# Optimization experiments

Measured on AMD Instinct MI355X. Metric: run time of the kernel, lower is better.

## Reference

```python
import jax, jax.numpy as jnp
import numpy as np

N_NODES = 100000
N_EDGES = 3200000
N_GRAPHS = 64
NEG_SLOPE = 0.2


def mish(x):
    return x * jnp.tanh(jax.nn.softplus(x))


def gat_layer(x, src, dst, W, b, a_src, a_dst, heads, out_ch, n_nodes):
    # h: [N, H, C]
    h = (x @ W).reshape(n_nodes, heads, out_ch)
    alpha_s = jnp.sum(h * a_src[None], axis=-1)  # [N, H]
    alpha_d = jnp.sum(h * a_dst[None], axis=-1)  # [N, H]
    e = jax.nn.leaky_relu(alpha_s[src] + alpha_d[dst], NEG_SLOPE)  # [E, H]
    # scatter-softmax over incoming edges of each destination node
    emax = jax.ops.segment_max(e, dst, num_segments=n_nodes)  # [N, H]
    ee = jnp.exp(e - emax[dst])
    den = jax.ops.segment_sum(ee, dst, num_segments=n_nodes)
    alpha = ee / (den[dst] + 1e-16)  # [E, H]
    msg = h[src] * alpha[..., None]  # [E, H, C]
    out = jax.ops.segment_sum(msg, dst, num_segments=n_nodes)
    return out.reshape(n_nodes, heads * out_ch) + b


def setup_inputs() -> dict:
    key = jax.random.key(0)
    ks = jax.random.split(key, 10)
    x = jax.random.normal(ks[0], (N_NODES, 128), dtype=jnp.float32)
    edge_index = jax.random.randint(ks[1], (2, N_EDGES), 0, N_NODES, dtype=jnp.int64)
    batch = jnp.sort(jax.random.randint(ks[2], (N_NODES,), 0, N_GRAPHS, dtype=jnp.int64))
    s1 = 1.0 / np.sqrt(128.0)
    s2 = 1.0 / np.sqrt(16.0)
    return {
        "x": x,
        "edge_index": edge_index,
        "batch": batch,
        "W1": jax.random.normal(ks[3], (128, 16), dtype=jnp.float32) * s1,
        "b1": jnp.zeros((16,), dtype=jnp.float32),
        "a_src1": jax.random.normal(ks[4], (4, 4), dtype=jnp.float32) * 0.5,
        "a_dst1": jax.random.normal(ks[5], (4, 4), dtype=jnp.float32) * 0.5,
        "W2": jax.random.normal(ks[6], (16, 32), dtype=jnp.float32) * s2,
        "b2": jnp.zeros((32,), dtype=jnp.float32),
        "a_src2": jax.random.normal(ks[7], (1, 32), dtype=jnp.float32) * 0.5,
        "a_dst2": jax.random.normal(ks[8], (1, 32), dtype=jnp.float32) * 0.5,
    }


def reference(x, edge_index, batch, W1, b1, a_src1, a_dst1, W2, b2, a_src2, a_dst2):
    n = x.shape[0]
    # PyG GATConv default add_self_loops=True
    loop = jnp.arange(n, dtype=edge_index.dtype)
    src = jnp.concatenate([edge_index[0], loop])
    dst = jnp.concatenate([edge_index[1], loop])
    h = mish(gat_layer(x, src, dst, W1, b1, a_src1, a_dst1, heads=4, out_ch=4, n_nodes=n))
    h = mish(gat_layer(h, src, dst, W2, b2, a_src2, a_dst2, heads=1, out_ch=32, n_nodes=n))
    # global_mean_pool
    sums = jax.ops.segment_sum(h, batch, num_segments=N_GRAPHS)
    cnts = jax.ops.segment_sum(jnp.ones((n,), h.dtype), batch, num_segments=N_GRAPHS)
    return sums / jnp.maximum(cnts, 1.0)[:, None]
```

## Files before the change

### kernel.cpp

```cpp
#include <hip/hip_runtime.h>
#include <hip/hip_fp16.h>
#include <math.h>

#define NEG_SLOPE 0.2f
#define GB 192
#define SB 320
#define CHMAX 11264
#define CAP 5120
#define CAPH 2560

typedef _Float16 half2v __attribute__((ext_vector_type(2)));
typedef _Float16 half4v __attribute__((ext_vector_type(4)));

__device__ __forceinline__ float mishf(float x) {
    if (x > 15.f) return x;
    float ex = __expf(x);
    float y = 1.f + ex;
    float y2 = y * y;
    return x * (y2 - 1.f) / (y2 + 1.f);
}

__device__ __forceinline__ float lw(float e) {
    return __expf(fmaxf(e, NEG_SLOPE * e));
}

__device__ __forceinline__ float hdot2a(half2v a, half2v b, float c) {
#if __has_builtin(__builtin_amdgcn_fdot2)
    return __builtin_amdgcn_fdot2(a, b, c, false);
#else
    return (float)a.x * (float)b.x + (float)a.y * (float)b.y + c;
#endif
}

__global__ __launch_bounds__(1024) void front_kernel(
        const float* __restrict__ x, const float* __restrict__ W1,
        const float* __restrict__ a_dst,
        const float* __restrict__ W2, const float* __restrict__ as2,
        const float* __restrict__ ad2,
        _Float16* __restrict__ hpre1h, float* __restrict__ addst,
        float* __restrict__ vs, float* __restrict__ vd,
        const int* __restrict__ src, const int* __restrict__ dst,
        int E, int Etot, int CH, int NB, int N, int NT,
        int* __restrict__ cursor, int* __restrict__ pairs) {
    __shared__ __attribute__((aligned(16))) char smem[63824];
    int tid = threadIdx.x;
    if (blockIdx.x < GB) {
        float* Wlt = (float*)smem;
        float* xs  = Wlt + 16 * 132;
        if (blockIdx.x == 0 && tid < 16) {
            float ps = 0.f, pd = 0.f;
            #pragma unroll
            for (int c = 0; c < 32; c++) {
                float w = W2[tid * 32 + c];
                ps += w * as2[c];
                pd += w * ad2[c];
            }
            vs[tid] = ps; vd[tid] = pd;
        }
        for (int i = tid; i < 2048; i += 1024) Wlt[(i & 15) * 132 + (i >> 4)] = W1[i];
        int nl = tid >> 4, ch = tid & 15;
        for (int t = blockIdx.x; t < NT; t += GB) {
            int nodebase = t * 64;
            int nvalid = min(64, N - nodebase);
            __syncthreads();
            const float4* x4 = (const float4*)(x + (size_t)nodebase * 128);
            #pragma unroll
            for (int u = 0; u < 2; u++) {
                int i = tid + (u << 10);
                int tnl = i >> 5;
                if (tnl < nvalid) {
                    float4 v = x4[i];
                    int k = (i & 31) * 4;
                    float* dp = &xs[tnl * 132 + k];
                    dp[0] = v.x; dp[1] = v.y; dp[2] = v.z; dp[3] = v.w;
                }
            }
            __syncthreads();
            if (nl < nvalid) {
                const float4* xr4 = (const float4*)&xs[nl * 132];
                const float4* wr4 = (const float4*)&Wlt[ch * 132];
                float acc = 0.f;
                #pragma unroll
                for (int k4 = 0; k4 < 32; k4++) {
                    float4 xv = xr4[k4];
                    float4 wv = wr4[k4];
                    acc += xv.x * wv.x + xv.y * wv.y + xv.z * wv.z + xv.w * wv.w;
                }
                int node = nodebase + nl;
                hpre1h[node * 16 + ch] = (_Float16)acc;
                float pd = acc * a_dst[ch];
                pd += __shfl_xor(pd, 1); pd += __shfl_xor(pd, 2);
                if ((ch & 3) == 0) addst[node * 4 + (ch >> 2)] = pd;
            }
        }
    } else {
        int nb2 = 2 * NB;
        int* A    = (int*)smem;
        int* Boff = A + nb2;
        int* C    = Boff + nb2;
        int* buf  = C + nb2;
        int blk = blockIdx.x - GB;
        for (int b = tid; b < nb2; b += 1024) A[b] = 0;
        __syncthreads();
        int ibeg = blk * CH, iend = min((blk + 1) * CH, Etot);
        int cdv[11], cs[11];
        #pragma unroll
        for (int u = 0; u < 11; u++) {
            int i = ibeg + tid + (u << 10);
            int d = -1, s = 0;
            if (i < iend) {
                if (i < E) { d = dst[i]; s = src[i]; } else { d = i - E; s = d; }
                atomicAdd(&A[d >> 6], 1);
            }
            cdv[u] = d; cs[u] = s;
        }
        for (int i = ibeg + CHMAX + tid; i < iend; i += 1024) {
            int d, s;
            if (i < E) { d = dst[i]; s = src[i]; } else { d = i - E; s = d; }
            int f = d >> 6;
            int pos = atomicAdd(&cursor[f], 1);
            pos = pos < CAPH ? pos : CAPH - 1;
            size_t addr = (size_t)(f >> 1) * CAP + ((f & 1) ? (CAP - 1 - pos) : pos);
            pairs[addr] = s | ((d & 63) << 17);
        }
        __syncthreads();
        for (int b = tid; b < nb2; b += 1024) Boff[b] = A[b];
        __syncthreads();
        for (int o = 1; o < nb2; o <<= 1) {
            int i1 = tid, i2 = tid + 1024;
            int v1 = 0, v2 = 0;
            if (i1 < nb2 && i1 >= o) v1 = Boff[i1 - o];
            if (i2 < nb2 && i2 >= o) v2 = Boff[i2 - o];
            __syncthreads();
            if (i1 < nb2) Boff[i1] += v1;
            if (i2 < nb2) Boff[i2] += v2;
            __syncthreads();
        }
        for (int b = tid; b < nb2; b += 1024) {
            int cnt = A[b];
            Boff[b] -= cnt;
            C[b] = cnt ? atomicAdd(&cursor[b], cnt) : 0;
        }
        __syncthreads();
        for (int b = tid; b < nb2; b += 1024) A[b] = 0;
        __syncthreads();
        #pragma unroll
        for (int u = 0; u < 11; u++) {
            int d = cdv[u];
            if (d < 0) continue;
            int f = d >> 6;
            int r = atomicAdd(&A[f], 1);
            buf[Boff[f] + r] = cs[u] | ((d & 63) << 17);
        }
        __syncthreads();
        int total = iend - ibeg;
        if (total > CHMAX) total = CHMAX;
        if (total < 0) total = 0;
        for (int j = tid; j < total; j += 1024) {
            int lo = 0, hi = nb2 - 1;
            while (lo < hi) {
                int mid = (lo + hi + 1) >> 1;
                if (Boff[mid] <= j) lo = mid; else hi = mid - 1;
            }
            int f = lo;
            int pos = C[f] + (j - Boff[f]);
            pos = pos < CAPH ? pos : CAPH - 1;
            size_t addr = (size_t)(f >> 1) * CAP + ((f & 1) ? (CAP - 1 - pos) : pos);
            pairs[addr] = buf[j];
        }
    }
}

__global__ __launch_bounds__(256) void csragg1_kernel(
        const int* __restrict__ pairs, const int* __restrict__ btotal,
        int NB, int N,
        int* __restrict__ ssorted, int* __restrict__ rs, int* __restrict__ re,
        const float* __restrict__ a_src1, const float* __restrict__ addst,
        const _Float16* __restrict__ hpre1h, const float* __restrict__ b1,
        const float* __restrict__ vs, const float* __restrict__ vd,
        _Float16* __restrict__ hpack,
        float* __restrict__ ad2n) {
    __shared__ int deg[64];
    __shared__ int s[64];
    __shared__ int cur[64];
    __shared__ __attribute__((aligned(16))) int lds_sorted[CAPH];
    int tid = threadIdx.x, bh = blockIdx.x;
    int B = bh >> 1, half = bh & 1;
    int nb0 = (B << 7) + (half << 6);
    int cnt_nodes = min(64, N - nb0);
    int c = min(btotal[bh], CAPH);
    int rbase = B * CAP + (half ? CAP - c : 0);
    if (tid < 64) deg[tid] = 0;
    __syncthreads();
    for (int j = tid; j < c; j += 256)
        atomicAdd(&deg[(pairs[rbase + j] >> 17) & 63], 1);
    __syncthreads();
    if (tid < 64) s[tid] = deg[tid];
    __syncthreads();
    for (int o = 1; o < 64; o <<= 1) {
        int v = 0;
        if (tid < 64 && tid >= o) v = s[tid - o];
        __syncthreads();
        if (tid < 64) s[tid] += v;
        __syncthreads();
    }
    if (tid < 64) {
        int ex = s[tid] - deg[tid];
        cur[tid] = ex;
        if (tid < cnt_nodes) {
            rs[nb0 + tid] = bh * CAPH + ex;
            re[nb0 + tid] = bh * CAPH + ex + deg[tid];
        }
    }
    __syncthreads();
    for (int j = tid; j < c; j += 256) {
        int p = pairs[rbase + j];
        int pos = atomicAdd(&cur[(p >> 17) & 63], 1);
        lds_sorted[pos < CAPH ? pos : CAPH - 1] = p & 0x1FFFF;
    }
    __syncthreads();

    {
        int t4 = c >> 2;
        const int4* ls4 = (const int4*)lds_sorted;
        int4* gs4 = (int4*)(ssorted + (size_t)bh * CAPH);
        for (int j = tid; j < t4; j += 256) gs4[j] = ls4[j];
        for (int j = (t4 << 2) + tid; j < c; j += 256)
            ssorted[(size_t)bh * CAPH + j] = lds_sorted[j];
    }

    int wave = tid >> 6;
    int lane = tid & 63;
    int head = lane & 3, er = lane >> 2;
    int c0 = head * 4;
    half2v w01, w23;
    w01.x = (_Float16)a_src1[c0];     w01.y = (_Float16)a_src1[c0 + 1];
    w23.x = (_Float16)a_src1[c0 + 2]; w23.y = (_Float16)a_src1[c0 + 3];
    for (int r = 0; r < 16; r++) {
        int ln = (wave << 4) + r;
        if (ln >= cnt_nodes) break;
        int node = nb0 + ln;
        int end = cur[ln];
        int start = end - deg[ln];
        float adh = addst[node * 4 + head];
        float den = 0.f, a0 = 0.f, a1 = 0.f, a2 = 0.f, a3 = 0.f;
        int last = end - 1;
        int jb = start;
        for (; jb + 32 <= end; jb += 32) {
            int s0 = lds_sorted[jb + er];
            int s1 = lds_sorted[jb + 16 + er];
            half4v h0 = *(const half4v*)(hpre1h + (size_t)s0 * 16 + c0);
            half4v h1 = *(const half4v*)(hpre1h + (size_t)s1 * 16 + c0);
            half2v h0lo = __builtin_shufflevector(h0, h0, 0, 1);
            half2v h0hi = __builtin_shufflevector(h0, h0, 2, 3);
            half2v h1lo = __builtin_shufflevector(h1, h1, 0, 1);
            half2v h1hi = __builtin_shufflevector(h1, h1, 2, 3);
            float p0 = hdot2a(h0lo, w01, hdot2a(h0hi, w23, 0.f));
            float p1 = hdot2a(h1lo, w01, hdot2a(h1hi, w23, 0.f));
            float wt0 = lw(p0 + adh);
            float wt1 = lw(p1 + adh);
            den += wt0 + wt1;
            a0 += (float)h0.x * wt0 + (float)h1.x * wt1;
            a1 += (float)h0.y * wt0 + (float)h1.y * wt1;
            a2 += (float)h0.z * wt0 + (float)h1.z * wt1;
            a3 += (float)h0.w * wt0 + (float)h1.w * wt1;
        }
        if (jb < end) {
            int j0 = jb + er, j1 = jb + 16 + er;
            int k0 = (j0 <= last) ? j0 : last;
            int k1 = (j1 <= last) ? j1 : last;
            int s0 = lds_sorted[k0];
            int s1 = lds_sorted[k1];
            half4v h0 = *(const half4v*)(hpre1h + (size_t)s0 * 16 + c0);
            half4v h1 = *(const half4v*)(hpre1h + (size_t)s1 * 16 + c0);
            half2v h0lo = __builtin_shufflevector(h0, h0, 0, 1);
            half2v h0hi = __builtin_shufflevector(h0, h0, 2, 3);
            half2v h1lo = __builtin_shufflevector(h1, h1, 0, 1);
            half2v h1hi = __builtin_shufflevector(h1, h1, 2, 3);
            float p0 = hdot2a(h0lo, w01, hdot2a(h0hi, w23, 0.f));
            float p1 = hdot2a(h1lo, w01, hdot2a(h1hi, w23, 0.f));
            float wt0 = (j0 <= last) ? lw(p0 + adh) : 0.f;
            float wt1 = (j1 <= last) ? lw(p1 + adh) : 0.f;
            den += wt0 + wt1;
            a0 += (float)h0.x * wt0 + (float)h1.x * wt1;
            a1 += (float)h0.y * wt0 + (float)h1.y * wt1;
            a2 += (float)h0.z * wt0 + (float)h1.z * wt1;
            a3 += (float)h0.w * wt0 + (float)h1.w * wt1;
        }
        a0 += __shfl_xor(a0, 4);  a1 += __shfl_xor(a1, 4);  a2 += __shfl_xor(a2, 4);  a3 += __shfl_xor(a3, 4);  den += __shfl_xor(den, 4);
        a0 += __shfl_xor(a0, 8);  a1 += __shfl_xor(a1, 8);  a2 += __shfl_xor(a2, 8);  a3 += __shfl_xor(a3, 8);  den += __shfl_xor(den, 8);
        a0 += __shfl_xor(a0, 16); a1 += __shfl_xor(a1, 16); a2 += __shfl_xor(a2, 16); a3 += __shfl_xor(a3, 16); den += __shfl_xor(den, 16);
        a0 += __shfl_xor(a0, 32); a1 += __shfl_xor(a1, 32); a2 += __shfl_xor(a2, 32); a3 += __shfl_xor(a3, 32); den += __shfl_xor(den, 32);
        if (er == 0) {
            float inv = 1.f / (den + 1e-16f);
            float o0 = mishf(a0 * inv + b1[c0]);
            float o1 = mishf(a1 * inv + b1[c0 + 1]);
            float o2 = mishf(a2 * inv + b1[c0 + 2]);
            float o3 = mishf(a3 * inv + b1[c0 + 3]);
            half4v oh;
            oh.x = (_Float16)o0; oh.y = (_Float16)o1;
            oh.z = (_Float16)o2; oh.w = (_Float16)o3;
            _Float16* rec = hpack + (size_t)node * 32;
            *(half4v*)(rec + c0) = oh;
            float ps = o0 * vs[c0] + o1 * vs[c0 + 1] + o2 * vs[c0 + 2] + o3 * vs[c0 + 3];
            float pd = o0 * vd[c0] + o1 * vd[c0 + 1] + o2 * vd[c0 + 2] + o3 * vd[c0 + 3];
            ps += __shfl_xor(ps, 1); pd += __shfl_xor(pd, 1);
            ps += __shfl_xor(ps, 2); pd += __shfl_xor(pd, 2);
            if (head == 0) {
                *(float*)(rec + 16) = ps;
                ad2n[node] = pd;
            }
        }
    }
}

__global__ void agg2_kernel(const int* __restrict__ rs, const int* __restrict__ re,
                            const int* __restrict__ ssorted,
                            const _Float16* __restrict__ hpack,
                            const float* __restrict__ ad2n,
                            float* __restrict__ agg16, float* __restrict__ denv, int N) {
    int wave = threadIdx.x >> 6;
    int lane = threadIdx.x & 63;
    int b = blockIdx.x;
    int xcd = b & 7, i = b >> 3;
    int f = xcd + ((i >> 4) << 3);
    int sub = i & 15;
    int node = f * 64 + sub * 4 + wave;
    if (node >= N) return;
    int start = rs[node], end = re[node];
    int q = lane & 3, er = lane >> 2;
    int c0 = q * 4;
    float adh = ad2n[node];
    float den = 0.f, a0 = 0.f, a1 = 0.f, a2 = 0.f, a3 = 0.f;
    int last = end - 1;
    int jb = start;
    for (; jb + 32 <= end; jb += 32) {
        int s0 = __builtin_nontemporal_load(ssorted + jb + er);
        int s1 = __builtin_nontemporal_load(ssorted + jb + 16 + er);
        const _Float16* r0 = hpack + (size_t)s0 * 32;
        const _Float16* r1 = hpack + (size_t)s1 * 32;
        float as0 = *(const float*)(r0 + 16);
        float as1 = *(const float*)(r1 + 16);
        half4v h0 = *(const half4v*)(r0 + c0);
        half4v h1 = *(const half4v*)(r1 + c0);
        float wt0 = lw(as0 + adh);
        float wt1 = lw(as1 + adh);
        den += wt0 + wt1;
        a0 += (float)h0.x * wt0 + (float)h1.x * wt1;
        a1 += (float)h0.y * wt0 + (float)h1.y * wt1;
        a2 += (float)h0.z * wt0 + (float)h1.z * wt1;
        a3 += (float)h0.w * wt0 + (float)h1.w * wt1;
    }
    if (jb < end) {
        int j0 = jb + er, j1 = jb + 16 + er;
        int k0 = (j0 <= last) ? j0 : last;
        int k1 = (j1 <= last) ? j1 : last;
        int s0 = __builtin_nontemporal_load(ssorted + k0);
        int s1 = __builtin_nontemporal_load(ssorted + k1);
        const _Float16* r0 = hpack + (size_t)s0 * 32;
        const _Float16* r1 = hpack + (size_t)s1 * 32;
        float as0 = *(const float*)(r0 + 16);
        float as1 = *(const float*)(r1 + 16);
        half4v h0 = *(const half4v*)(r0 + c0);
        half4v h1 = *(const half4v*)(r1 + c0);
        float wt0 = (j0 <= last) ? lw(as0 + adh) : 0.f;
        float wt1 = (j1 <= last) ? lw(as1 + adh) : 0.f;
        den += wt0 + wt1;
        a0 += (float)h0.x * wt0 + (float)h1.x * wt1;
        a1 += (float)h0.y * wt0 + (float)h1.y * wt1;
        a2 += (float)h0.z * wt0 + (float)h1.z * wt1;
        a3 += (float)h0.w * wt0 + (float)h1.w * wt1;
    }
    a0 += __shfl_xor(a0, 4);  a1 += __shfl_xor(a1, 4);  a2 += __shfl_xor(a2, 4);  a3 += __shfl_xor(a3, 4);  den += __shfl_xor(den, 4);
    a0 += __shfl_xor(a0, 8);  a1 += __shfl_xor(a1, 8);  a2 += __shfl_xor(a2, 8);  a3 += __shfl_xor(a3, 8);  den += __shfl_xor(den, 8);
    a0 += __shfl_xor(a0, 16); a1 += __shfl_xor(a1, 16); a2 += __shfl_xor(a2, 16); a3 += __shfl_xor(a3, 16); den += __shfl_xor(den, 16);
    a0 += __shfl_xor(a0, 32); a1 += __shfl_xor(a1, 32); a2 += __shfl_xor(a2, 32); a3 += __shfl_xor(a3, 32); den += __shfl_xor(den, 32);
    if (er == 0) {
        float4 o; o.x = a0; o.y = a1; o.z = a2; o.w = a3;
        *(float4*)(agg16 + (size_t)node * 16 + c0) = o;
        if (q == 0) denv[node] = den;
    }
}

__global__ void post2pool_kernel(const float* __restrict__ agg16, const float* __restrict__ denv,
                                 const float* __restrict__ W2, const float* __restrict__ b2,
                                 const int* __restrict__ batch,
                                 float* __restrict__ pool, float* __restrict__ cnt, int N) {
    __shared__ float Wl[16 * 32];
    int tid = threadIdx.x;
    for (int i = tid; i < 512; i += 256) Wl[i] = W2[i];
    __syncthreads();
    int r = tid >> 5, ch = tid & 31;
    float bc = b2[ch];
    int base = blockIdx.x * 128;
    int cur = -1;
    float sum = 0.f, c = 0.f;
    for (int it = 0; it < 16; it++) {
        int n = base + it * 8 + r;
        if (n >= N) break;
        int g = batch[n];
        if (g != cur) {
            if (cur >= 0) {
                atomicAdd(&pool[cur * 32 + ch], sum);
                if (ch == 0) atomicAdd(&cnt[cur], c);
            }
            cur = g; sum = 0.f; c = 0.f;
        }
        const float* ar = agg16 + (size_t)n * 16;
        float acc = 0.f;
        #pragma unroll
        for (int k = 0; k < 16; k++) acc += ar[k] * Wl[k * 32 + ch];
        float val = mishf(acc / (denv[n] + 1e-16f) + bc);
        sum += val;
        c += 1.f;
    }
    if (cur >= 0) {
        atomicAdd(&pool[cur * 32 + ch], sum);
        if (ch == 0) atomicAdd(&cnt[cur], c);
    }
}

__global__ void fin_kernel(const float* __restrict__ pool, const float* __restrict__ cnt,
                           float* __restrict__ out, int NG) {
    int i = blockIdx.x * blockDim.x + threadIdx.x;
    if (i >= NG * 32) return;
    out[i] = pool[i] / fmaxf(cnt[i >> 5], 1.0f);
}

extern "C" void kernel_launch(void* const* d_in, const int* in_sizes, int n_in,
                              void* d_out, int out_size, void* d_ws, size_t ws_size,
                              hipStream_t stream) {
    const float* x   = (const float*)d_in[0];
    const int* eidx  = (const int*)d_in[1];
    const int* batch = (const int*)d_in[2];
    const float* W1  = (const float*)d_in[3];
    const float* b1  = (const float*)d_in[4];
    const float* as1 = (const float*)d_in[5];
    const float* ad1 = (const float*)d_in[6];
    const float* W2  = (const float*)d_in[7];
    const float* b2  = (const float*)d_in[8];
    const float* as2 = (const float*)d_in[9];
    const float* ad2 = (const float*)d_in[10];
    float* out = (float*)d_out;

    int N = in_sizes[0] / 128;
    int E = in_sizes[1] / 2;
    int Etot = E + N;
    int NG = out_size / 32;
    const int* esrc = eidx;
    const int* edst = eidx + E;

    int NB = (N + 127) >> 7;
    int NBH = NB * 2;
    int NT = (N + 63) >> 6;
    int CH = (Etot + SB - 1) / SB;

    char* p = (char*)d_ws;
    auto alloc = [&](size_t nbytes) {
        p = (char*)(((uintptr_t)p + 15) & ~(uintptr_t)15);
        void* r = (void*)p; p += nbytes; return r;
    };
    int* pairs        = (int*)alloc((size_t)NB * CAP * 4);
    int* ssorted      = (int*)alloc((size_t)NBH * CAPH * 4);
    int* rs           = (int*)alloc((size_t)N * 4);
    int* re           = (int*)alloc((size_t)N * 4);
    int* cursor       = (int*)alloc((size_t)NBH * 4);
    _Float16* hpre1h  = (_Float16*)alloc((size_t)N * 16 * 2);
    _Float16* hpack   = (_Float16*)alloc((size_t)N * 64);
    float* addst1  = (float*)alloc((size_t)N * 4 * 4);
    float* ad2n    = (float*)alloc((size_t)N * 4);
    float* agg16   = (float*)alloc((size_t)N * 16 * 4);
    float* denv    = (float*)alloc((size_t)N * 4);
    float* vs      = (float*)alloc(16 * 4);
    float* vd      = (float*)alloc(16 * 4);
    float* pool    = (float*)alloc((size_t)NG * 32 * 4);
    float* cnt     = (float*)alloc((size_t)NG * 4);

    hipMemsetAsync(cursor, 0, (size_t)NBH * 4, stream);
    hipMemsetAsync(pool, 0, (size_t)NG * 32 * 4, stream);
    hipMemsetAsync(cnt, 0, (size_t)NG * 4, stream);

    front_kernel<<<GB + SB, 1024, 0, stream>>>(x, W1, ad1, W2, as2, ad2,
                                               hpre1h, addst1, vs, vd,
                                               esrc, edst, E, Etot, CH, NB, N, NT,
                                               cursor, pairs);
    csragg1_kernel<<<NBH, 256, 0, stream>>>(pairs, cursor, NB, N,
                                            ssorted, rs, re, as1, addst1, hpre1h,
                                            b1, vs, vd, hpack, ad2n);
    int NF = ((NBH + 7) >> 3) << 3;
    agg2_kernel<<<NF * 16, 256, 0, stream>>>(rs, re, ssorted, hpack, ad2n,
                                             agg16, denv, N);
    post2pool_kernel<<<(N + 127) / 128, 256, 0, stream>>>(agg16, denv, W2, b2, batch,
                                                          pool, cnt, N);
    fin_kernel<<<(NG * 32 + 255) / 256, 256, 0, stream>>>(pool, cnt, out, NG);
}
```

Before: 334.6 us.

## Fuse layer-2 aggregation with projection and pooling; split packed node record

Merges the layer-2 edge aggregation and the W2 projection/mish/mean-pool into one kernel, so per-node aggregates and denominators stay in LDS and no longer round-trip through global memory. The packed 64-byte node record (16 halves plus a float score) becomes a 32-byte half array and a separate float array for the source scores. Each block now handles 64 nodes with each wave looping over 16 nodes, which cuts the grid from about 25k blocks to about 1.6k and drops the XCD-aware block remapping. The gather now touches two arrays per edge instead of one record, and there are fewer waves to hide gather latency.

```diff
diff --git a/kernel.cpp b/kernel.cpp
--- a/kernel.cpp
+++ b/kernel.cpp
@@ -178,8 +178,8 @@
         const float* __restrict__ a_src1, const float* __restrict__ addst,
         const _Float16* __restrict__ hpre1h, const float* __restrict__ b1,
         const float* __restrict__ vs, const float* __restrict__ vd,
-        _Float16* __restrict__ hpack,
-        float* __restrict__ ad2n) {
+        _Float16* __restrict__ hpost1h,
+        float* __restrict__ as2n, float* __restrict__ ad2n) {
     __shared__ int deg[64];
     __shared__ int s[64];
     __shared__ int cur[64];
@@ -300,123 +300,120 @@
             half4v oh;
             oh.x = (_Float16)o0; oh.y = (_Float16)o1;
             oh.z = (_Float16)o2; oh.w = (_Float16)o3;
-            _Float16* rec = hpack + (size_t)node * 32;
-            *(half4v*)(rec + c0) = oh;
+            *(half4v*)(hpost1h + (size_t)node * 16 + c0) = oh;
             float ps = o0 * vs[c0] + o1 * vs[c0 + 1] + o2 * vs[c0 + 2] + o3 * vs[c0 + 3];
             float pd = o0 * vd[c0] + o1 * vd[c0 + 1] + o2 * vd[c0 + 2] + o3 * vd[c0 + 3];
             ps += __shfl_xor(ps, 1); pd += __shfl_xor(pd, 1);
             ps += __shfl_xor(ps, 2); pd += __shfl_xor(pd, 2);
-            if (head == 0) {
-                *(float*)(rec + 16) = ps;
-                ad2n[node] = pd;
-            }
-        }
-    }
-}
-
-__global__ void agg2_kernel(const int* __restrict__ rs, const int* __restrict__ re,
-                            const int* __restrict__ ssorted,
-                            const _Float16* __restrict__ hpack,
-                            const float* __restrict__ ad2n,
-                            float* __restrict__ agg16, float* __restrict__ denv, int N) {
-    int wave = threadIdx.x >> 6;
-    int lane = threadIdx.x & 63;
-    int b = blockIdx.x;
-    int xcd = b & 7, i = b >> 3;
-    int f = xcd + ((i >> 4) << 3);
-    int sub = i & 15;
-    int node = f * 64 + sub * 4 + wave;
-    if (node >= N) return;
-    int start = rs[node], end = re[node];
+            if (head == 0) { as2n[node] = ps; ad2n[node] = pd; }
+        }
+    }
+}
+
+__global__ __launch_bounds__(256) void agg2pool_kernel(
+        const int* __restrict__ rs, const int* __restrict__ re,
+        const int* __restrict__ ssorted,
+        const float* __restrict__ as2n, const float* __restrict__ ad2n,
+        const _Float16* __restrict__ hpost1h,
+        const float* __restrict__ W2, const float* __restrict__ b2,
+        const int* __restrict__ batch,
+        float* __restrict__ pool, float* __restrict__ cntg, int N) {
+    __shared__ float W2l[512];
+    __shared__ float lds_agg[64 * 17];
+    __shared__ float lds_den[64];
+    int tid = threadIdx.x, bh = blockIdx.x;
+    int nb0 = bh << 6;
+    int cnt_nodes = min(64, N - nb0);
+    if (cnt_nodes <= 0) return;
+    for (int i = tid; i < 512; i += 256) W2l[i] = W2[i];
+
+    int wave = tid >> 6;
+    int lane = tid & 63;
     int q = lane & 3, er = lane >> 2;
     int c0 = q * 4;
-    float adh = ad2n[node];
-    float den = 0.f, a0 = 0.f, a1 = 0.f, a2 = 0.f, a3 = 0.f;
-    int last = end - 1;
-    int jb = start;
-    for (; jb + 32 <= end; jb += 32) {
-        int s0 = __builtin_nontemporal_load(ssorted + jb + er);
-        int s1 = __builtin_nontemporal_load(ssorted + jb + 16 + er);
-        const _Float16* r0 = hpack + (size_t)s0 * 32;
-        const _Float16* r1 = hpack + (size_t)s1 * 32;
-        float as0 = *(const float*)(r0 + 16);
-        float as1 = *(const float*)(r1 + 16);
-        half4v h0 = *(const half4v*)(r0 + c0);
-        half4v h1 = *(const half4v*)(r1 + c0);
-        float wt0 = lw(as0 + adh);
-        float wt1 = lw(as1 + adh);
-        den += wt0 + wt1;
-        a0 += (float)h0.x * wt0 + (float)h1.x * wt1;
-        a1 += (float)h0.y * wt0 + (float)h1.y * wt1;
-        a2 += (float)h0.z * wt0 + (float)h1.z * wt1;
-        a3 += (float)h0.w * wt0 + (float)h1.w * wt1;
-    }
-    if (jb < end) {
-        int j0 = jb + er, j1 = jb + 16 + er;
-        int k0 = (j0 <= last) ? j0 : last;
-        int k1 = (j1 <= last) ? j1 : last;
-        int s0 = __builtin_nontemporal_load(ssorted + k0);
-        int s1 = __builtin_nontemporal_load(ssorted + k1);
-        const _Float16* r0 = hpack + (size_t)s0 * 32;
-        const _Float16* r1 = hpack + (size_t)s1 * 32;
-        float as0 = *(const float*)(r0 + 16);
-        float as1 = *(const float*)(r1 + 16);
-        half4v h0 = *(const half4v*)(r0 + c0);
-        half4v h1 = *(const half4v*)(r1 + c0);
-        float wt0 = (j0 <= last) ? lw(as0 + adh) : 0.f;
-        float wt1 = (j1 <= last) ? lw(as1 + adh) : 0.f;
-        den += wt0 + wt1;
-        a0 += (float)h0.x * wt0 + (float)h1.x * wt1;
-        a1 += (float)h0.y * wt0 + (float)h1.y * wt1;
-        a2 += (float)h0.z * wt0 + (float)h1.z * wt1;
-        a3 += (float)h0.w * wt0 + (float)h1.w * wt1;
-    }
-    a0 += __shfl_xor(a0, 4);  a1 += __shfl_xor(a1, 4);  a2 += __shfl_xor(a2, 4);  a3 += __shfl_xor(a3, 4);  den += __shfl_xor(den, 4);
-    a0 += __shfl_xor(a0, 8);  a1 += __shfl_xor(a1, 8);  a2 += __shfl_xor(a2, 8);  a3 += __shfl_xor(a3, 8);  den += __shfl_xor(den, 8);
-    a0 += __shfl_xor(a0, 16); a1 += __shfl_xor(a1, 16); a2 += __shfl_xor(a2, 16); a3 += __shfl_xor(a3, 16); den += __shfl_xor(den, 16);
-    a0 += __shfl_xor(a0, 32); a1 += __shfl_xor(a1, 32); a2 += __shfl_xor(a2, 32); a3 += __shfl_xor(a3, 32); den += __shfl_xor(den, 32);
-    if (er == 0) {
-        float4 o; o.x = a0; o.y = a1; o.z = a2; o.w = a3;
-        *(float4*)(agg16 + (size_t)node * 16 + c0) = o;
-        if (q == 0) denv[node] = den;
-    }
-}
-
-__global__ void post2pool_kernel(const float* __restrict__ agg16, const float* __restrict__ denv,
-                                 const float* __restrict__ W2, const float* __restrict__ b2,
-                                 const int* __restrict__ batch,
-                                 float* __restrict__ pool, float* __restrict__ cnt, int N) {
-    __shared__ float Wl[16 * 32];
-    int tid = threadIdx.x;
-    for (int i = tid; i < 512; i += 256) Wl[i] = W2[i];
-    __syncthreads();
-    int r = tid >> 5, ch = tid & 31;
+    const _Float16* hb = hpost1h + c0;
+
+    for (int r = 0; r < 16; r++) {
+        int ln = (wave << 4) + r;
+        if (ln >= cnt_nodes) break;
+        int node = nb0 + ln;
+        int start = rs[node], end = re[node];
+        float adh = ad2n[node];
+        float den = 0.f, a0 = 0.f, a1 = 0.f, a2 = 0.f, a3 = 0.f;
+        int last = end - 1;
+        int jb = start;
+        for (; jb + 32 <= end; jb += 32) {
+            int s0 = __builtin_nontemporal_load(ssorted + jb + er);
+            int s1 = __builtin_nontemporal_load(ssorted + jb + 16 + er);
+            float e0 = as2n[s0] + adh;
+            float e1 = as2n[s1] + adh;
+            half4v h0 = *(const half4v*)(hb + (size_t)s0 * 16);
+            half4v h1 = *(const half4v*)(hb + (size_t)s1 * 16);
+            float wt0 = lw(e0);
+            float wt1 = lw(e1);
+            den += wt0 + wt1;
+            a0 += (float)h0.x * wt0 + (float)h1.x * wt1;
+            a1 += (float)h0.y * wt0 + (float)h1.y * wt1;
+            a2 += (float)h0.z * wt0 + (float)h1.z * wt1;
+            a3 += (float)h0.w * wt0 + (float)h1.w * wt1;
+        }
+        if (jb < end) {
+            int j0 = jb + er, j1 = jb + 16 + er;
+            int k0 = (j0 <= last) ? j0 : last;
+            int k1 = (j1 <= last) ? j1 : last;
+            int s0 = __builtin_nontemporal_load(ssorted + k0);
+            int s1 = __builtin_nontemporal_load(ssorted + k1);
+            float e0 = as2n[s0] + adh;
+            float e1 = as2n[s1] + adh;
+            half4v h0 = *(const half4v*)(hb + (size_t)s0 * 16);
+            half4v h1 = *(const half4v*)(hb + (size_t)s1 * 16);
+            float wt0 = (j0 <= last) ? lw(e0) : 0.f;
+            float wt1 = (j1 <= last) ? lw(e1) : 0.f;
+            den += wt0 + wt1;
+            a0 += (float)h0.x * wt0 + (float)h1.x * wt1;
+            a1 += (float)h0.y * wt0 + (float)h1.y * wt1;
+            a2 += (float)h0.z * wt0 + (float)h1.z * wt1;
+            a3 += (float)h0.w * wt0 + (float)h1.w * wt1;
+        }
+        a0 += __shfl_xor(a0, 4);  a1 += __shfl_xor(a1, 4);  a2 += __shfl_xor(a2, 4);  a3 += __shfl_xor(a3, 4);  den += __shfl_xor(den, 4);
+        a0 += __shfl_xor(a0, 8);  a1 += __shfl_xor(a1, 8);  a2 += __shfl_xor(a2, 8);  a3 += __shfl_xor(a3, 8);  den += __shfl_xor(den, 8);
+        a0 += __shfl_xor(a0, 16); a1 += __shfl_xor(a1, 16); a2 += __shfl_xor(a2, 16); a3 += __shfl_xor(a3, 16); den += __shfl_xor(den, 16);
+        a0 += __shfl_xor(a0, 32); a1 += __shfl_xor(a1, 32); a2 += __shfl_xor(a2, 32); a3 += __shfl_xor(a3, 32); den += __shfl_xor(den, 32);
+        if (er == 0) {
+            float* ag = &lds_agg[ln * 17 + c0];
+            ag[0] = a0; ag[1] = a1; ag[2] = a2; ag[3] = a3;
+            if (q == 0) lds_den[ln] = den;
+        }
+    }
+    __syncthreads();
+
+    int rr = tid >> 5, ch = tid & 31;
     float bc = b2[ch];
-    int base = blockIdx.x * 128;
-    int cur = -1;
-    float sum = 0.f, c = 0.f;
-    for (int it = 0; it < 16; it++) {
-        int n = base + it * 8 + r;
-        if (n >= N) break;
+    int curg = -1;
+    float sum = 0.f, cc = 0.f;
+    for (int it = 0; it < 8; it++) {
+        int ln = it * 8 + rr;
+        if (ln >= cnt_nodes) break;
+        int n = nb0 + ln;
         int g = batch[n];
-        if (g != cur) {
-            if (cur >= 0) {
-                atomicAdd(&pool[cur * 32 + ch], sum);
-                if (ch == 0) atomicAdd(&cnt[cur], c);
-            }
-            cur = g; sum = 0.f; c = 0.f;
-        }
-        const float* ar = agg16 + (size_t)n * 16;
+        if (g != curg) {
+            if (curg >= 0) {
+                atomicAdd(&pool[curg * 32 + ch], sum);
+                if (ch == 0) atomicAdd(&cntg[curg], cc);
+            }
+            curg = g; sum = 0.f; cc = 0.f;
+        }
+        const float* ar = &lds_agg[ln * 17];
         float acc = 0.f;
         #pragma unroll
-        for (int k = 0; k < 16; k++) acc += ar[k] * Wl[k * 32 + ch];
-        float val = mishf(acc / (denv[n] + 1e-16f) + bc);
+        for (int k = 0; k < 16; k++) acc += ar[k] * W2l[k * 32 + ch];
+        float val = mishf(acc / (lds_den[ln] + 1e-16f) + bc);
         sum += val;
-        c += 1.f;
-    }
-    if (cur >= 0) {
-        atomicAdd(&pool[cur * 32 + ch], sum);
-        if (ch == 0) atomicAdd(&cnt[cur], c);
+        cc += 1.f;
+    }
+    if (curg >= 0) {
+        atomicAdd(&pool[curg * 32 + ch], sum);
+        if (ch == 0) atomicAdd(&cntg[curg], cc);
     }
 }
 
@@ -466,11 +463,10 @@
     int* re           = (int*)alloc((size_t)N * 4);
     int* cursor       = (int*)alloc((size_t)NBH * 4);
     _Float16* hpre1h  = (_Float16*)alloc((size_t)N * 16 * 2);
-    _Float16* hpack   = (_Float16*)alloc((size_t)N * 64);
+    _Float16* hpost1h = (_Float16*)alloc((size_t)N * 16 * 2);
     float* addst1  = (float*)alloc((size_t)N * 4 * 4);
+    float* as2n    = (float*)alloc((size_t)N * 4);
     float* ad2n    = (float*)alloc((size_t)N * 4);
-    float* agg16   = (float*)alloc((size_t)N * 16 * 4);
-    float* denv    = (float*)alloc((size_t)N * 4);
     float* vs      = (float*)alloc(16 * 4);
     float* vd      = (float*)alloc(16 * 4);
     float* pool    = (float*)alloc((size_t)NG * 32 * 4);
@@ -486,11 +482,8 @@
                                                cursor, pairs);
     csragg1_kernel<<<NBH, 256, 0, stream>>>(pairs, cursor, NB, N,
                                             ssorted, rs, re, as1, addst1, hpre1h,
-                                            b1, vs, vd, hpack, ad2n);
-    int NF = ((NBH + 7) >> 3) << 3;
-    agg2_kernel<<<NF * 16, 256, 0, stream>>>(rs, re, ssorted, hpack, ad2n,
-                                             agg16, denv, N);
-    post2pool_kernel<<<(N + 127) / 128, 256, 0, stream>>>(agg16, denv, W2, b2, batch,
-                                                          pool, cnt, N);
+                                            b1, vs, vd, hpost1h, as2n, ad2n);
+    agg2pool_kernel<<<NBH, 256, 0, stream>>>(rs, re, ssorted, as2n, ad2n, hpost1h,
+                                             W2, b2, batch, pool, cnt, N);
     fin_kernel<<<(NG * 32 + 255) / 256, 256, 0, stream>>>(pool, cnt, out, NG);
 }
```

Measured after the change: 363.3 us. +8.6%, slower.
